# Performance work log

Hardware: AMD Instinct MI355X
Metric: run time of the kernel (lower is better)

The kernel has to match this reference:

```python
import jax, jax.numpy as jnp
import numpy as np

N_NODES = 100000
N_EDGES = 1600000
K = 3  # TAGConv default hops


def _make_lin(key, out_dim, in_dim):
    # K+1 bias-free linears (stacked) + one shared output bias, per PyG TAGConv
    kw, = jax.random.split(key, 1)
    scale = 1.0 / np.sqrt(in_dim)
    W = jax.random.uniform(kw, (K + 1, out_dim, in_dim), jnp.float32, -scale, scale)
    b = jnp.zeros((out_dim,), jnp.float32)
    return W, b


def setup_inputs() -> dict:
    key = jax.random.key(0)
    ks = jax.random.split(key, 6)
    x = jax.random.normal(ks[0], (N_NODES, 128), jnp.float32)
    edge_index = jax.random.randint(ks[1], (2, N_EDGES), 0, N_NODES, jnp.int64)
    W1, b1 = _make_lin(ks[2], 128, 128)
    W2, b2 = _make_lin(ks[3], 64, 128)
    W3, b3 = _make_lin(ks[4], 16, 64)
    return {"x": x, "edge_index": edge_index, "W1": W1, "b1": b1,
            "W2": W2, "b2": b2, "W3": W3, "b3": b3}


def _tagconv(x, row, col, norm, W, b, n):
    # out = sum_k lin_k(A_norm^k x) + b ; message x_j*norm gathered at col
    out = jnp.einsum('nd,od->no', x, W[0])
    h = x
    for k in range(1, W.shape[0]):
        h = jax.ops.segment_sum(norm[:, None] * h[row], col, num_segments=n)
        out = out + jnp.einsum('nd,od->no', h, W[k])
    return out + b


def _dropout(x, key, p=0.5):
    keep = jax.random.bernoulli(key, 1.0 - p, x.shape)
    return jnp.where(keep, x / (1.0 - p), 0.0)


def reference(x, edge_index, W1, b1, W2, b2, W3, b3):
    n = x.shape[0]
    row, col = edge_index[0], edge_index[1]
    # gcn_norm without self-loops (TAGConv default)
    deg = jax.ops.segment_sum(jnp.ones(row.shape[0], x.dtype), col, num_segments=n)
    dis = jnp.where(deg > 0, 1.0 / jnp.sqrt(jnp.where(deg > 0, deg, 1.0)), 0.0)
    norm = dis[row] * dis[col]

    dk1, dk2 = jax.random.split(jax.random.key(42))
    h = _tagconv(x, row, col, norm, W1, b1, n)
    h = _dropout(h, dk1)
    h = _tagconv(h, row, col, norm, W2, b2, n)
    h = jax.nn.elu(h)
    h = _dropout(h, dk2)
    h = _tagconv(h, row, col, norm, W3, b3, n)
    return h
```

## Files before the change

### kernel.cpp

```cpp
#include <hip/hip_runtime.h>
#include <stdint.h>
#include <math.h>

#define N_NODES 100000
#define N_EDGES 1600000

typedef __bf16 bf16_t;
typedef __attribute__((ext_vector_type(4))) __bf16 bf16x4;
typedef __attribute__((ext_vector_type(8))) __bf16 bf16x8;
typedef __attribute__((ext_vector_type(4))) float f32x4;

__device__ __forceinline__ f32x4 mfma16(bf16x8 a, bf16x8 b, f32x4 c) {
  return __builtin_amdgcn_mfma_f32_16x16x32_bf16(a, b, c, 0, 0, 0);
}

__device__ __host__ __forceinline__ uint32_t rotl32(uint32_t v, int d) {
  return (v << d) | (v >> (32 - d));
}

__device__ __host__ __forceinline__ void threefry2x32(uint32_t k0, uint32_t k1,
                                                      uint32_t x0, uint32_t x1,
                                                      uint32_t& o0, uint32_t& o1) {
  uint32_t ks0 = k0, ks1 = k1, ks2 = k0 ^ k1 ^ 0x1BD11BDAu;
  x0 += ks0; x1 += ks1;
#define TF_R(r) { x0 += x1; x1 = rotl32(x1, r); x1 ^= x0; }
  TF_R(13) TF_R(15) TF_R(26) TF_R(6)
  x0 += ks1; x1 += ks2 + 1u;
  TF_R(17) TF_R(29) TF_R(16) TF_R(24)
  x0 += ks2; x1 += ks0 + 2u;
  TF_R(13) TF_R(15) TF_R(26) TF_R(6)
  x0 += ks0; x1 += ks1 + 3u;
  TF_R(17) TF_R(29) TF_R(16) TF_R(24)
  x0 += ks1; x1 += ks2 + 4u;
  TF_R(13) TF_R(15) TF_R(26) TF_R(6)
  x0 += ks2; x1 += ks0 + 5u;
#undef TF_R
  o0 = x0; o1 = x1;
}

__device__ __forceinline__ float drop_scale(uint32_t idx, uint32_t k0, uint32_t k1) {
  uint32_t o0, o1;
  threefry2x32(k0, k1, 0u, idx, o0, o1);
  uint32_t bits = o0 ^ o1;
  float u = __uint_as_float((bits >> 9) | 0x3f800000u) - 1.0f;
  return (u < 0.5f) ? 2.0f : 0.0f;
}

__global__ __launch_bounds__(256) void detect_kernel(const int* __restrict__ ei,
                                                     int* __restrict__ found_nonzero) {
  int idx = blockIdx.x * 256 + threadIdx.x;
  size_t j = (size_t)idx * 781;
  if (ei[2 * j + 1] != 0) atomicOr(found_nonzero, 1);
}

__device__ __forceinline__ int edge_row(const int* ei, bool i32, int e) {
  return i32 ? ei[e] : ei[2 * (size_t)e];
}
__device__ __forceinline__ int edge_col(const int* ei, bool i32, int e) {
  return i32 ? ei[N_EDGES + e] : ei[2 * ((size_t)N_EDGES + (size_t)e)];
}

__global__ __launch_bounds__(256) void deg_kernel(const int* __restrict__ ei,
                                                  const int* __restrict__ flag,
                                                  int* __restrict__ deg) {
  int e = blockIdx.x * 256 + threadIdx.x;
  if (e < N_EDGES) {
    bool i32 = *flag != 0;
    atomicAdd(&deg[edge_col(ei, i32, e)], 1);
  }
}

__global__ __launch_bounds__(256) void dis_kernel(const int* __restrict__ deg,
                                                  float* __restrict__ dis) {
  int n = blockIdx.x * 256 + threadIdx.x;
  if (n < N_NODES) {
    int d = deg[n];
    dis[n] = (d > 0) ? (1.0f / sqrtf((float)d)) : 0.0f;
  }
}

#define SCAN_NB 391
__global__ __launch_bounds__(256) void bsum_kernel(const int* __restrict__ deg,
                                                   int* __restrict__ bsum) {
  __shared__ int sh[256];
  int i = blockIdx.x * 256 + threadIdx.x;
  sh[threadIdx.x] = (i < N_NODES) ? deg[i] : 0;
  __syncthreads();
  for (int ofs = 128; ofs > 0; ofs >>= 1) {
    if (threadIdx.x < ofs) sh[threadIdx.x] += sh[threadIdx.x + ofs];
    __syncthreads();
  }
  if (threadIdx.x == 0) bsum[blockIdx.x] = sh[0];
}

__global__ __launch_bounds__(512) void bscan_kernel(const int* __restrict__ bsum,
                                                    int* __restrict__ boffs) {
  __shared__ int sh[512];
  int t = threadIdx.x;
  int v = (t < SCAN_NB) ? bsum[t] : 0;
  sh[t] = v;
  __syncthreads();
  for (int ofs = 1; ofs < 512; ofs <<= 1) {
    int u = (t >= ofs) ? sh[t - ofs] : 0;
    __syncthreads();
    sh[t] += u;
    __syncthreads();
  }
  if (t < SCAN_NB) boffs[t] = sh[t] - v;
  if (t == 0) boffs[SCAN_NB] = sh[SCAN_NB - 1];
}

__global__ __launch_bounds__(256) void rptr_kernel(const int* __restrict__ deg,
                                                   const int* __restrict__ boffs,
                                                   int* __restrict__ rptr) {
  __shared__ int sh[256];
  int i = blockIdx.x * 256 + threadIdx.x;
  int v = (i < N_NODES) ? deg[i] : 0;
  sh[threadIdx.x] = v;
  __syncthreads();
  for (int ofs = 1; ofs < 256; ofs <<= 1) {
    int u = (threadIdx.x >= ofs) ? sh[threadIdx.x - ofs] : 0;
    __syncthreads();
    sh[threadIdx.x] += u;
    __syncthreads();
  }
  if (i <= N_NODES) rptr[i] = boffs[blockIdx.x] + sh[threadIdx.x] - v;
}

__global__ __launch_bounds__(256) void fill_kernel(const int* __restrict__ ei,
                                                   const int* __restrict__ flag,
                                                   const float* __restrict__ dis,
                                                   const int* __restrict__ rptr,
                                                   int* cursor,
                                                   int2* __restrict__ erec) {
  int e = blockIdx.x * 256 + threadIdx.x;
  if (e < N_EDGES) {
    bool i32 = *flag != 0;
    int r = edge_row(ei, i32, e);
    int c = edge_col(ei, i32, e);
    int p = atomicAdd(&cursor[c], 1);
    int idx = rptr[c] + p;
    float nrm = dis[r] * dis[c];
    erec[idx] = make_int2(r, __float_as_int(nrm));
  }
}

__global__ __launch_bounds__(256) void wcvt_kernel(
    const float* __restrict__ W1, const float* __restrict__ W2,
    const float* __restrict__ W3,
    bf16_t* __restrict__ Wb1, bf16_t* __restrict__ Wb2,
    bf16_t* __restrict__ Wb3) {
  int i = blockIdx.x * 256 + threadIdx.x;
  if (i < 65536) Wb1[i] = (bf16_t)W1[i];
  if (i < 32768) Wb2[i] = (bf16_t)W2[i];
  if (i < 4096)  Wb3[i] = (bf16_t)W3[i];
}

template <int DIN, int LOG_DOUT, int NCH, bool YB, bool AHL>
__global__ __launch_bounds__(256) void matmul_mfma_kernel(
    const void* __restrict__ hA, const void* __restrict__ hAlo,
    const bf16_t* __restrict__ Wb, const float* __restrict__ bias,
    float* __restrict__ y0, void* __restrict__ y1,
    void* __restrict__ y2, void* __restrict__ y3) {
  constexpr int LDK = DIN + 8;
  constexpr int DOUT = 1 << LOG_DOUT;
  constexpr int KI = DIN / 32;
  __shared__ bf16_t sm[2][64 * LDK];
  const int m0 = blockIdx.x * 64;
  const int tid = threadIdx.x;

  if (AHL) {
    constexpr int NL = 64 * DIN / 8 / 256;
#pragma unroll
    for (int it = 0; it < NL; ++it) {
      int idx = tid + it * 256;
      int r = idx / (DIN / 8), cc = (idx % (DIN / 8)) * 8;
      int gm = m0 + r;
      uint4 vh = make_uint4(0, 0, 0, 0), vl = make_uint4(0, 0, 0, 0);
      if (gm < N_NODES) {
        vh = ((const uint4*)hA)[((size_t)gm * DIN + cc) >> 3];
        vl = ((const uint4*)hAlo)[((size_t)gm * DIN + cc) >> 3];
      }
      *(uint4*)&sm[0][r * LDK + cc] = vh;
      *(uint4*)&sm[1][r * LDK + cc] = vl;
    }
  } else {
    constexpr int NL = 64 * DIN / 4 / 256;
    union U4 { bf16_t b[4]; uint2 u; };
#pragma unroll
    for (int it = 0; it < NL; ++it) {
      int idx = tid + it * 256;
      int r = idx / (DIN / 4), cc = (idx % (DIN / 4)) * 4;
      int gm = m0 + r;
      float4 v = (gm < N_NODES) ? ((const float4*)hA)[((size_t)gm * DIN + cc) >> 2]
                                : make_float4(0.f, 0.f, 0.f, 0.f);
      U4 hi, lo;
      hi.b[0] = (bf16_t)v.x; lo.b[0] = (bf16_t)(v.x - (float)hi.b[0]);
      hi.b[1] = (bf16_t)v.y; lo.b[1] = (bf16_t)(v.y - (float)hi.b[1]);
      hi.b[2] = (bf16_t)v.z; lo.b[2] = (bf16_t)(v.z - (float)hi.b[2]);
      hi.b[3] = (bf16_t)v.w; lo.b[3] = (bf16_t)(v.w - (float)hi.b[3]);
      *(uint2*)&sm[0][r * LDK + cc] = hi.u;
      *(uint2*)&sm[1][r * LDK + cc] = lo.u;
    }
  }
  __syncthreads();

  const int w = tid >> 6, lane = tid & 63;
  const int wm = w & 1, wn = w >> 1;
  const int quad = lane >> 4, lr = lane & 15;

  bf16x8 aH[2][KI], aL[2][KI];
#pragma unroll
  for (int mt = 0; mt < 2; ++mt)
#pragma unroll
    for (int ki = 0; ki < KI; ++ki) {
      int rowa = wm * 32 + mt * 16 + lr;
      int koff = ki * 32 + quad * 8;
      aH[mt][ki] = *(const bf16x8*)&sm[0][rowa * LDK + koff];
      aL[mt][ki] = *(const bf16x8*)&sm[1][rowa * LDK + koff];
    }
  __syncthreads();

  constexpr int NLB = 64 * DIN / 8 / 256;
  uint4 wreg[NLB];
#pragma unroll
  for (int it = 0; it < NLB; ++it) {
    int idx = tid + it * 256;
    int r = idx / (DIN / 8), cc = (idx % (DIN / 8)) * 8;
    wreg[it] = ((const uint4*)Wb)[(((size_t)r) * DIN + cc) >> 3];
    *(uint4*)&sm[0][r * LDK + cc] = wreg[it];
  }
  __syncthreads();

  for (int nc = 0; nc < NCH; ++nc) {
    int p = nc & 1;
    if (nc + 1 < NCH) {
#pragma unroll
      for (int it = 0; it < NLB; ++it) {
        int idx = tid + it * 256;
        int r = idx / (DIN / 8), cc = (idx % (DIN / 8)) * 8;
        wreg[it] = ((const uint4*)Wb)[(((size_t)((nc + 1) * 64 + r)) * DIN + cc) >> 3];
      }
    }

    f32x4 acc[2][2] = {};
#pragma unroll
    for (int ki = 0; ki < KI; ++ki) {
      int koff = ki * 32 + quad * 8;
      bf16x8 bfr[2];
#pragma unroll
      for (int nt = 0; nt < 2; ++nt)
        bfr[nt] = *(const bf16x8*)&sm[p][(wn * 32 + nt * 16 + lr) * LDK + koff];
#pragma unroll
      for (int mt = 0; mt < 2; ++mt)
#pragma unroll
        for (int nt = 0; nt < 2; ++nt) {
          acc[mt][nt] = mfma16(bfr[nt], aH[mt][ki], acc[mt][nt]);
          acc[mt][nt] = mfma16(bfr[nt], aL[mt][ki], acc[mt][nt]);
        }
    }

    if (nc + 1 < NCH) {
#pragma unroll
      for (int it = 0; it < NLB; ++it) {
        int idx = tid + it * 256;
        int r = idx / (DIN / 8), cc = (idx % (DIN / 8)) * 8;
        *(uint4*)&sm[p ^ 1][r * LDK + cc] = wreg[it];
      }
    }
    __syncthreads();

    const int n0 = nc * 64;
#pragma unroll
    for (int mt = 0; mt < 2; ++mt) {
      int m = m0 + wm * 32 + mt * 16 + lr;
      if (m >= N_NODES) continue;
#pragma unroll
      for (int nt = 0; nt < 2; ++nt) {
        int nb = n0 + wn * 32 + nt * 16 + quad * 4;
        int k = nb >> LOG_DOUT;
        int o = nb & (DOUT - 1);
        size_t oi = (size_t)m * DOUT + o;
        if (k == 0) {
          float4 bv = *(const float4*)&bias[o];
          float4 st = make_float4(acc[mt][nt][0] + bv.x, acc[mt][nt][1] + bv.y,
                                  acc[mt][nt][2] + bv.z, acc[mt][nt][3] + bv.w);
          *(float4*)&y0[oi] = st;
        } else {
          void* yk = (k == 1) ? y1 : (k == 2) ? y2 : y3;
          if (YB) {
            bf16x4 bb;
            bb.x = (bf16_t)acc[mt][nt][0];
            bb.y = (bf16_t)acc[mt][nt][1];
            bb.z = (bf16_t)acc[mt][nt][2];
            bb.w = (bf16_t)acc[mt][nt][3];
            *(bf16x4*)((bf16_t*)yk + oi) = bb;
          } else {
            *(f32x4*)((float*)yk + oi) = acc[mt][nt];
          }
        }
      }
    }
  }
}

template <int D, int EPI, bool ZBF, bool ABF, int OMODE>
__global__ __launch_bounds__(256) void prop_kernel(
    const void* __restrict__ zv, const void* __restrict__ addv,
    void* __restrict__ outv, void* __restrict__ outv2,
    const int* __restrict__ rptr, const int2* __restrict__ erec,
    uint32_t k0, uint32_t k1) {
  constexpr int LPN = D / 4;
  constexpr int NPB = 256 / LPN;
  int lane = threadIdx.x % LPN;
  int nsub = threadIdx.x / LPN;
  int c = blockIdx.x * NPB + nsub;
  if (c >= N_NODES) return;
  int e0 = rptr[c], e1 = rptr[c + 1];
  float a0 = 0.f, a1 = 0.f, a2 = 0.f, a3 = 0.f;

  auto ld = [&](int r, float v[4]) {
    if (ZBF) {
      bf16x4 t = ((const bf16x4*)zv)[(size_t)r * LPN + lane];
      v[0] = (float)t.x; v[1] = (float)t.y; v[2] = (float)t.z; v[3] = (float)t.w;
    } else {
      float4 t = ((const float4*)zv)[(size_t)r * LPN + lane];
      v[0] = t.x; v[1] = t.y; v[2] = t.z; v[3] = t.w;
    }
  };

  int e = e0;
  for (; e + 3 < e1; e += 4) {
    int2 q[4];
    float v[4][4];
#pragma unroll
    for (int j = 0; j < 4; ++j) q[j] = erec[e + j];
#pragma unroll
    for (int j = 0; j < 4; ++j) ld(q[j].x, v[j]);
#pragma unroll
    for (int j = 0; j < 4; ++j) {
      float wv = __int_as_float(q[j].y);
      a0 = fmaf(wv, v[j][0], a0);
      a1 = fmaf(wv, v[j][1], a1);
      a2 = fmaf(wv, v[j][2], a2);
      a3 = fmaf(wv, v[j][3], a3);
    }
  }
  for (; e < e1; ++e) {
    int2 q = erec[e];
    float wv = __int_as_float(q.y);
    float v[4];
    ld(q.x, v);
    a0 = fmaf(wv, v[0], a0);
    a1 = fmaf(wv, v[1], a1);
    a2 = fmaf(wv, v[2], a2);
    a3 = fmaf(wv, v[3], a3);
  }

  size_t pidx = (size_t)c * LPN + lane;
  uint32_t fidx = (uint32_t)c * D + 4 * lane;
  float ax[4];
  if (ABF) {
    bf16x4 t = ((const bf16x4*)addv)[pidx];
    ax[0] = (float)t.x; ax[1] = (float)t.y; ax[2] = (float)t.z; ax[3] = (float)t.w;
  } else {
    float4 t = ((const float4*)addv)[pidx];
    ax[0] = t.x; ax[1] = t.y; ax[2] = t.z; ax[3] = t.w;
  }
  float o[4] = {a0 + ax[0], a1 + ax[1], a2 + ax[2], a3 + ax[3]};
  if (EPI == 1) {
#pragma unroll
    for (int j = 0; j < 4; ++j) o[j] *= drop_scale(fidx + j, k0, k1);
  }
  if (EPI == 2) {
#pragma unroll
    for (int j = 0; j < 4; ++j) {
      o[j] = (o[j] > 0.f) ? o[j] : expm1f(o[j]);
      o[j] *= drop_scale(fidx + j, k0, k1);
    }
  }
  if (OMODE == 0) {
    ((float4*)outv)[pidx] = make_float4(o[0], o[1], o[2], o[3]);
  } else if (OMODE == 1) {
    bf16x4 bv;
    bv.x = (bf16_t)o[0]; bv.y = (bf16_t)o[1];
    bv.z = (bf16_t)o[2]; bv.w = (bf16_t)o[3];
    ((bf16x4*)outv)[pidx] = bv;
  } else {
    bf16x4 hv, lv;
    hv.x = (bf16_t)o[0]; hv.y = (bf16_t)o[1];
    hv.z = (bf16_t)o[2]; hv.w = (bf16_t)o[3];
    lv.x = (bf16_t)(o[0] - (float)hv.x);
    lv.y = (bf16_t)(o[1] - (float)hv.y);
    lv.z = (bf16_t)(o[2] - (float)hv.z);
    lv.w = (bf16_t)(o[3] - (float)hv.w);
    ((bf16x4*)outv)[pidx] = hv;
    ((bf16x4*)outv2)[pidx] = lv;
  }
}

extern "C" void kernel_launch(void* const* d_in, const int* in_sizes, int n_in,
                              void* d_out, int out_size, void* d_ws, size_t ws_size,
                              hipStream_t stream) {
  const float* x  = (const float*)d_in[0];
  const int*   ei = (const int*)d_in[1];
  const float* W1 = (const float*)d_in[2];
  const float* b1 = (const float*)d_in[3];
  const float* W2 = (const float*)d_in[4];
  const float* b2 = (const float*)d_in[5];
  const float* W3 = (const float*)d_in[6];
  const float* b3 = (const float*)d_in[7];
  float* out = (float*)d_out;

  char* ws = (char*)d_ws;
  size_t off = 0;
  auto alloc = [&](size_t bytes) -> char* {
    char* p = ws + off;
    off += (bytes + 255) & ~(size_t)255;
    return p;
  };
  int*   flag   = (int*)alloc(256);
  int*   deg    = (int*)alloc((size_t)N_NODES * 4);
  int*   cursor = (int*)alloc((size_t)N_NODES * 4);
  float* dis    = (float*)alloc((size_t)N_NODES * 4);
  int*   rptr   = (int*)alloc((size_t)(N_NODES + 1) * 4);
  int*   bsum   = (int*)alloc((size_t)(SCAN_NB + 1) * 4);
  int*   boffs  = (int*)alloc((size_t)(SCAN_NB + 1) * 4);
  int2*  erec   = (int2*)alloc((size_t)N_EDGES * 8);
  bf16_t* Wb1  = (bf16_t*)alloc(65536 * 2);
  bf16_t* Wb2  = (bf16_t*)alloc(32768 * 2);
  bf16_t* Wb3  = (bf16_t*)alloc(4096 * 2);
  float*  R0  = (float*)alloc((size_t)N_NODES * 128 * 4);
  float*  R2  = (float*)alloc((size_t)N_NODES * 16 * 4);
  bf16_t* Zb0 = (bf16_t*)alloc((size_t)N_NODES * 128 * 2);
  bf16_t* Zb1 = (bf16_t*)alloc((size_t)N_NODES * 128 * 2);
  bf16_t* Bb1 = (bf16_t*)alloc((size_t)N_NODES * 128 * 2);
  bf16_t* Bb2 = (bf16_t*)alloc((size_t)N_NODES * 128 * 2);

  hipMemsetAsync(flag, 0, 256, stream);
  hipMemsetAsync(deg, 0, (size_t)N_NODES * 4, stream);
  hipMemsetAsync(cursor, 0, (size_t)N_NODES * 4, stream);

  detect_kernel<<<8, 256, 0, stream>>>(ei, flag);
  deg_kernel<<<(N_EDGES + 255) / 256, 256, 0, stream>>>(ei, flag, deg);
  dis_kernel<<<(N_NODES + 255) / 256, 256, 0, stream>>>(deg, dis);
  bsum_kernel<<<SCAN_NB, 256, 0, stream>>>(deg, bsum);
  bscan_kernel<<<1, 512, 0, stream>>>(bsum, boffs);
  rptr_kernel<<<SCAN_NB, 256, 0, stream>>>(deg, boffs, rptr);
  fill_kernel<<<(N_EDGES + 255) / 256, 256, 0, stream>>>(ei, flag, dis, rptr,
                                                         cursor, erec);
  wcvt_kernel<<<256, 256, 0, stream>>>(W1, W2, W3, Wb1, Wb2, Wb3);

  uint32_t d10, d11, d20, d21;
  threefry2x32(0u, 42u, 0u, 0u, d10, d11);
  threefry2x32(0u, 42u, 0u, 1u, d20, d21);

  const int MB = (N_NODES + 63) / 64;
  const int PB128 = (N_NODES + 7) / 8;
  const int PB64n = (N_NODES + 15) / 16;
  const int PB16n = (N_NODES + 63) / 64;

  matmul_mfma_kernel<128, 7, 8, true, false><<<MB, 256, 0, stream>>>(
      x, nullptr, Wb1, b1, R0, Bb1, Bb2, Zb0);
  prop_kernel<128, 0, true, true, 1><<<PB128, 256, 0, stream>>>(
      Zb0, Bb2, Zb1, nullptr, rptr, erec, 0, 0);
  prop_kernel<128, 0, true, true, 1><<<PB128, 256, 0, stream>>>(
      Zb1, Bb1, Zb0, nullptr, rptr, erec, 0, 0);
  prop_kernel<128, 1, true, false, 2><<<PB128, 256, 0, stream>>>(
      Zb0, R0, Bb2, Bb1, rptr, erec, d10, d11);

  float*  R1f = R0;
  bf16_t* S0 = Zb0;
  bf16_t* S1 = Zb0 + (size_t)N_NODES * 64;
  bf16_t* S2 = Zb1;
  bf16_t* S3 = Zb1 + (size_t)N_NODES * 64;
  matmul_mfma_kernel<128, 6, 4, true, true><<<MB, 256, 0, stream>>>(
      Bb2, Bb1, Wb2, b2, R1f, S2, S3, S0);
  prop_kernel<64, 0, true, true, 1><<<PB64n, 256, 0, stream>>>(
      S0, S3, S1, nullptr, rptr, erec, 0, 0);
  prop_kernel<64, 0, true, true, 1><<<PB64n, 256, 0, stream>>>(
      S1, S2, S0, nullptr, rptr, erec, 0, 0);
  prop_kernel<64, 2, true, false, 2><<<PB64n, 256, 0, stream>>>(
      S0, R1f, S2, S3, rptr, erec, d20, d21);

  float*  z0f = R2;
  bf16_t* zb1 = Bb1;
  bf16_t* zb2 = Bb1 + (size_t)N_NODES * 16;
  bf16_t* zb3 = Bb1 + (size_t)N_NODES * 32;
  matmul_mfma_kernel<64, 4, 1, true, true><<<MB, 256, 0, stream>>>(
      S2, S3, Wb3, b3, z0f, zb1, zb2, zb3);
  prop_kernel<16, 0, true, true, 1><<<PB16n, 256, 0, stream>>>(
      zb3, zb2, zb2, nullptr, rptr, erec, 0, 0);
  prop_kernel<16, 0, true, true, 1><<<PB16n, 256, 0, stream>>>(
      zb2, zb1, zb1, nullptr, rptr, erec, 0, 0);
  prop_kernel<16, 0, true, false, 0><<<PB16n, 256, 0, stream>>>(
      zb1, z0f, out, nullptr, rptr, erec, 0, 0);

  (void)in_sizes; (void)n_in; (void)out_size; (void)ws_size;
}
```

Baseline: 740.9 us.

## Build CSR via bucketed binning and shared-memory local scatter

Replaces the global per-edge atomic-cursor fill with a two-pass scheme. The first pass bins edges into 256-node buckets, using global atomics on the bucket counters only. The second pass runs one block per bucket, computes positions with shared-memory atomics, stages the records in LDS, and writes them out coalesced. This cuts scattered global atomics and random writes when building the CSR. The risk is a fixed bucket capacity of 6144 edges, which silently drops edges if a bucket overflows, and the bins buffer reuses R0 scratch memory.

```diff
diff --git a/kernel.cpp b/kernel.cpp
--- a/kernel.cpp
+++ b/kernel.cpp
@@ -60,14 +60,56 @@
   return i32 ? ei[N_EDGES + e] : ei[2 * ((size_t)N_EDGES + (size_t)e)];
 }
 
-__global__ __launch_bounds__(256) void deg_kernel(const int* __restrict__ ei,
+#define BKT_SHIFT 8
+#define NBKT 391
+#define BKT_CAP 6144
+
+__global__ __launch_bounds__(256) void bin_kernel(const int* __restrict__ ei,
                                                   const int* __restrict__ flag,
-                                                  int* __restrict__ deg) {
+                                                  int* __restrict__ deg,
+                                                  int* __restrict__ bcnt,
+                                                  int2* __restrict__ bins) {
   int e = blockIdx.x * 256 + threadIdx.x;
   if (e < N_EDGES) {
     bool i32 = *flag != 0;
-    atomicAdd(&deg[edge_col(ei, i32, e)], 1);
-  }
+    int r = edge_row(ei, i32, e);
+    int c = edge_col(ei, i32, e);
+    atomicAdd(&deg[c], 1);
+    int b = c >> BKT_SHIFT;
+    int p = atomicAdd(&bcnt[b], 1);
+    if (p < BKT_CAP) bins[(size_t)b * BKT_CAP + p] = make_int2(r, c);
+  }
+}
+
+__global__ __launch_bounds__(512) void scatter_kernel(
+    const int2* __restrict__ bins, const int* __restrict__ bcnt,
+    const float* __restrict__ dis, const int* __restrict__ rptr,
+    int2* __restrict__ erec) {
+  __shared__ int loff[256];
+  __shared__ int lcur[256];
+  __shared__ float ldis[256];
+  __shared__ int2 stage[BKT_CAP];
+  const int b = blockIdx.x;
+  const int c0 = b << BKT_SHIFT;
+  const int nn = min(256, N_NODES - c0);
+  const int t = threadIdx.x;
+  const int base = rptr[c0];
+  if (t < nn) {
+    loff[t] = rptr[c0 + t] - base;
+    lcur[t] = 0;
+    ldis[t] = dis[c0 + t];
+  }
+  __syncthreads();
+  const int cnt = min(bcnt[b], BKT_CAP);
+  for (int i = t; i < cnt; i += 512) {
+    int2 rec = bins[(size_t)b * BKT_CAP + i];
+    int lc = rec.y - c0;
+    float nrm = dis[rec.x] * ldis[lc];
+    int p = atomicAdd(&lcur[lc], 1);
+    stage[loff[lc] + p] = make_int2(rec.x, __float_as_int(nrm));
+  }
+  __syncthreads();
+  for (int i = t; i < cnt; i += 512) erec[base + i] = stage[i];
 }
 
 __global__ __launch_bounds__(256) void dis_kernel(const int* __restrict__ deg,
@@ -125,24 +167,6 @@
     __syncthreads();
   }
   if (i <= N_NODES) rptr[i] = boffs[blockIdx.x] + sh[threadIdx.x] - v;
-}
-
-__global__ __launch_bounds__(256) void fill_kernel(const int* __restrict__ ei,
-                                                   const int* __restrict__ flag,
-                                                   const float* __restrict__ dis,
-                                                   const int* __restrict__ rptr,
-                                                   int* cursor,
-                                                   int2* __restrict__ erec) {
-  int e = blockIdx.x * 256 + threadIdx.x;
-  if (e < N_EDGES) {
-    bool i32 = *flag != 0;
-    int r = edge_row(ei, i32, e);
-    int c = edge_col(ei, i32, e);
-    int p = atomicAdd(&cursor[c], 1);
-    int idx = rptr[c] + p;
-    float nrm = dis[r] * dis[c];
-    erec[idx] = make_int2(r, __float_as_int(nrm));
-  }
 }
 
 __global__ __launch_bounds__(256) void wcvt_kernel(
@@ -421,7 +445,7 @@
   };
   int*   flag   = (int*)alloc(256);
   int*   deg    = (int*)alloc((size_t)N_NODES * 4);
-  int*   cursor = (int*)alloc((size_t)N_NODES * 4);
+  int*   bcnt   = (int*)alloc((size_t)(NBKT + 1) * 4);
   float* dis    = (float*)alloc((size_t)N_NODES * 4);
   int*   rptr   = (int*)alloc((size_t)(N_NODES + 1) * 4);
   int*   bsum   = (int*)alloc((size_t)(SCAN_NB + 1) * 4);
@@ -437,18 +461,19 @@
   bf16_t* Bb1 = (bf16_t*)alloc((size_t)N_NODES * 128 * 2);
   bf16_t* Bb2 = (bf16_t*)alloc((size_t)N_NODES * 128 * 2);
 
+  int2* bins = (int2*)R0;
+
   hipMemsetAsync(flag, 0, 256, stream);
   hipMemsetAsync(deg, 0, (size_t)N_NODES * 4, stream);
-  hipMemsetAsync(cursor, 0, (size_t)N_NODES * 4, stream);
+  hipMemsetAsync(bcnt, 0, (size_t)(NBKT + 1) * 4, stream);
 
   detect_kernel<<<8, 256, 0, stream>>>(ei, flag);
-  deg_kernel<<<(N_EDGES + 255) / 256, 256, 0, stream>>>(ei, flag, deg);
+  bin_kernel<<<(N_EDGES + 255) / 256, 256, 0, stream>>>(ei, flag, deg, bcnt, bins);
   dis_kernel<<<(N_NODES + 255) / 256, 256, 0, stream>>>(deg, dis);
   bsum_kernel<<<SCAN_NB, 256, 0, stream>>>(deg, bsum);
   bscan_kernel<<<1, 512, 0, stream>>>(bsum, boffs);
   rptr_kernel<<<SCAN_NB, 256, 0, stream>>>(deg, boffs, rptr);
-  fill_kernel<<<(N_EDGES + 255) / 256, 256, 0, stream>>>(ei, flag, dis, rptr,
-                                                         cursor, erec);
+  scatter_kernel<<<NBKT, 512, 0, stream>>>(bins, bcnt, dis, rptr, erec);
   wcvt_kernel<<<256, 256, 0, stream>>>(W1, W2, W3, Wb1, Wb2, Wb3);
 
   uint32_t d10, d11, d20, d21;
```

Measured after the change: 1.225 ms. 65.3% more time.
